# Kernel tuning notes

Measured on AMD Instinct MI355X. Metric: run time of the kernel, lower is better.

## Reference

```python
import jax, jax.numpy as jnp
import numpy as np

B, S, IN_DIM, P_DIM, H = 2, 2048, 1024, 512, 8
HD = P_DIM // H
N_PENTA = 1024
SCALES = (128, 256, 512)
K_NEIGH = max(16, min(int(S * 0.15), 128))  # adaptive window -> 128
SCALE = 1.0 / float(np.sqrt(HD))
EPS = 1e-5


def _ln(x, g, b):
    mu = jnp.mean(x, axis=-1, keepdims=True)
    var = jnp.mean((x - mu) ** 2, axis=-1, keepdims=True)
    return (x - mu) * jax.lax.rsqrt(var + EPS) * g + b


def setup_inputs() -> dict:
    key = jax.random.key(0)
    ks = list(jax.random.split(key, 6 + 2 * len(SCALES)))
    w = lambda k, shp: jax.random.normal(k, shp, jnp.float32) * 0.02
    inp = {
        'sequence_features': jax.random.normal(ks[0], (B, S, IN_DIM), jnp.float32),
        'shared_pentachora': jax.random.normal(ks[1], (N_PENTA, 5, P_DIM), jnp.float32),
        'shared_positions': jax.random.uniform(ks[2], (N_PENTA,), dtype=jnp.float32),
        'proj_W': w(ks[3], (IN_DIM, P_DIM)), 'proj_b': jnp.zeros((P_DIM,), jnp.float32),
        'ln_g': jnp.ones((P_DIM,), jnp.float32), 'ln_b': jnp.zeros((P_DIM,), jnp.float32),
        'qkv_W': w(ks[4], (P_DIM, 3 * P_DIM)), 'qkv_b': jnp.zeros((3 * P_DIM,), jnp.float32),
        'out_W': w(ks[5], (P_DIM, P_DIM)), 'out_b': jnp.zeros((P_DIM,), jnp.float32),
    }
    i = 6
    for s in SCALES:
        inp[f'w1_{s}'] = w(ks[i], (P_DIM, 2 * s)); inp[f'b1_{s}'] = jnp.zeros((2 * s,), jnp.float32)
        inp[f'g_{s}'] = jnp.ones((2 * s,), jnp.float32); inp[f'bb_{s}'] = jnp.zeros((2 * s,), jnp.float32)
        inp[f'w2_{s}'] = w(ks[i + 1], (2 * s, s)); inp[f'b2_{s}'] = jnp.zeros((s,), jnp.float32)
        i += 2
    return inp


def _attend_one(z_b, pos_b, qkv_W, qkv_b, out_W, out_b):
    # z_b: [S, P_DIM], pos_b: [S]
    qkv = (z_b @ qkv_W + qkv_b).reshape(S, 3, H, HD)
    q = jnp.transpose(qkv[:, 0], (1, 0, 2))  # [H, S, HD]
    k = jnp.transpose(qkv[:, 1], (1, 0, 2))
    v = jnp.transpose(qkv[:, 2], (1, 0, 2))
    dist = jnp.abs(pos_b[:, None] - pos_b[None, :])  # [S, S]
    _, routes = jax.lax.top_k(-dist, K_NEIGH)        # [S, K] nearest in Cantor space
    kg = k[:, routes, :]  # [H, S, K, HD] gathered keys
    vg = v[:, routes, :]
    scores = jnp.einsum('hqd,hqkd->hqk', q, kg) * SCALE
    attn = jax.nn.softmax(scores, axis=-1)
    out = jnp.einsum('hqk,hqkd->hqd', attn, vg)
    out = jnp.transpose(out, (1, 0, 2)).reshape(S, P_DIM)
    return out @ out_W + out_b


def reference(sequence_features, shared_pentachora, shared_positions, proj_W, proj_b, ln_g, ln_b, qkv_W, qkv_b, out_W, out_b, w1_128, b1_128, g_128, bb_128, w2_128, b2_128, w1_256, b1_256, g_256, bb_256, w2_256, b2_256, w1_512, b1_512, g_512, bb_512, w2_512, b2_512):
    # centroids from pentachora vertices, L2-normalized
    cent = shared_pentachora.mean(axis=1)
    cent = cent / jnp.clip(jnp.linalg.norm(cent, axis=-1, keepdims=True), 1e-12)
    # input projection -> LN -> GELU -> L2 normalize
    z = jax.nn.gelu(_ln(sequence_features @ proj_W + proj_b, ln_g, ln_b), approximate=False)
    z = z / jnp.clip(jnp.linalg.norm(z, axis=-1, keepdims=True), 1e-12)
    # match to opinion anchors, inherit Cantor positions
    anchor_ids = jnp.argmax(jnp.einsum('bnd,pd->bnp', z, cent), axis=-1)  # [B, S]
    cantor_positions = shared_positions[anchor_ids]  # [B, S]
    # per-sample geometric sparse attention (vmapped over batch)
    z_att = jax.vmap(_attend_one, in_axes=(0, 0, None, None, None, None))(
        z, cantor_positions, qkv_W, qkv_b, out_W, out_b)  # [B, S, P_DIM]
    pooled = z_att.mean(axis=1)  # [B, P_DIM] (no attention mask)
    scale_params = (
        (w1_128, b1_128, g_128, bb_128, w2_128, b2_128),
        (w1_256, b1_256, g_256, bb_256, w2_256, b2_256),
        (w1_512, b1_512, g_512, bb_512, w2_512, b2_512),
    )
    outs = []
    for (w1, b1, g, bb, w2, b2) in scale_params:
        h = jax.nn.gelu(_ln(pooled @ w1 + b1, g, bb), approximate=False)
        outs.append(h @ w2 + b2)
    return jnp.concatenate(outs, axis=-1)  # [B, 128+256+512] concatenated scale opinions
```

## Files before the change

### kernel.cpp

```cpp
#include <hip/hip_runtime.h>
#include <math.h>

#define DEV __device__ __forceinline__

static constexpr int S_LEN  = 2048;
static constexpr int IN_DIM = 1024;
static constexpr int P_DIM  = 512;
static constexpr int NHEAD  = 8;
static constexpr int HD     = 64;
static constexpr int KN     = 128;

typedef __attribute__((ext_vector_type(8))) short bf16x8;
typedef __attribute__((ext_vector_type(4))) float f32x4;

DEV float gelu_exact(float x) {
    return 0.5f * x * (1.0f + erff(x * 0.70710678118654752440f));
}

DEV short bf_hi(float x) {
    unsigned u = __float_as_uint(x);
    unsigned r = (u + 0x7fffu + ((u >> 16) & 1u)) >> 16;
    return (short)r;
}
DEV float bf_f(short h) { return __uint_as_float(((unsigned)(unsigned short)h) << 16); }

DEV float block_reduce_sum(float v, float* sm4) {
    #pragma unroll
    for (int off = 32; off; off >>= 1) v += __shfl_down(v, off, 64);
    int lane = threadIdx.x & 63, w = threadIdx.x >> 6;
    __syncthreads();
    if (lane == 0) sm4[w] = v;
    __syncthreads();
    return sm4[0] + sm4[1] + sm4[2] + sm4[3];
}

DEV float wave_sum(float v) {
    #pragma unroll
    for (int off = 32; off; off >>= 1) v += __shfl_xor(v, off, 64);
    return v;
}

DEV void wt_body(const float* __restrict__ W, short* __restrict__ WTh,
                 short* __restrict__ WTl, int K, int N, int bk, int bn,
                 float (*tile)[65]) {
    int t = threadIdx.x;
    int c = t & 63, r4 = t >> 6;
    #pragma unroll
    for (int i = 0; i < 16; i++) {
        int row = r4 + i * 4;
        tile[row][c] = W[(long)(bk * 64 + row) * N + bn * 64 + c];
    }
    __syncthreads();
    #pragma unroll
    for (int i = 0; i < 16; i++) {
        int n = r4 + i * 4;
        float v = tile[c][n];
        short h = bf_hi(v);
        long o = (long)(bn * 64 + n) * K + bk * 64 + c;
        WTh[o] = h;
        WTl[o] = bf_hi(v - bf_f(h));
    }
}

DEV void t32_body(const float* __restrict__ W, float* __restrict__ WT,
                  int K, int N, int bk, int bn, float (*tile)[65]) {
    int t = threadIdx.x;
    int c = t & 63, r4 = t >> 6;
    #pragma unroll
    for (int i = 0; i < 16; i++) {
        int row = r4 + i * 4;
        tile[row][c] = W[(long)(bk * 64 + row) * N + bn * 64 + c];
    }
    __syncthreads();
    #pragma unroll
    for (int i = 0; i < 16; i++) {
        int n = r4 + i * 4;
        WT[(long)(bn * 64 + n) * K + bk * 64 + c] = tile[c][n];
    }
}

__global__ __launch_bounds__(256) void k_prep(const float* __restrict__ penta,
                                              short* __restrict__ ch, short* __restrict__ cl,
                                              const float* __restrict__ projW,
                                              short* __restrict__ pjh, short* __restrict__ pjl,
                                              const float* __restrict__ qkvW,
                                              short* __restrict__ qkh, short* __restrict__ qkl,
                                              const float* __restrict__ seq,
                                              short* __restrict__ sh, short* __restrict__ sl,
                                              unsigned long long* __restrict__ rowkey,
                                              float* __restrict__ pooledZ,
                                              const float* __restrict__ outW, float* __restrict__ outWT,
                                              const float* __restrict__ w1_0,
                                              const float* __restrict__ w1_1,
                                              const float* __restrict__ w1_2, float* __restrict__ w1T,
                                              const float* __restrict__ w2_0,
                                              const float* __restrict__ w2_1,
                                              const float* __restrict__ w2_2, float* __restrict__ w2T) {
    __shared__ float tile[64][65];
    __shared__ float sm4[4];
    int blk = blockIdx.x, t = threadIdx.x;
    if (blk < 1024) {
        int p = blk;
        if (t < 4) rowkey[p * 4 + t] = 0ull;
        if (p < 4) pooledZ[p * 256 + t] = 0.f;
        float c0 = 0.f, c1 = 0.f;
        #pragma unroll
        for (int v = 0; v < 5; v++) {
            const float* row = penta + ((long)p * 5 + v) * P_DIM;
            c0 += row[t];
            c1 += row[t + 256];
        }
        c0 /= 5.0f; c1 /= 5.0f;
        float tot = block_reduce_sum(c0 * c0 + c1 * c1, sm4);
        float n = fmaxf(sqrtf(tot), 1e-12f);
        float v0 = c0 / n, v1 = c1 / n;
        short h0 = bf_hi(v0), h1 = bf_hi(v1);
        ch[p * P_DIM + t]       = h0;
        ch[p * P_DIM + t + 256] = h1;
        cl[p * P_DIM + t]       = bf_hi(v0 - bf_f(h0));
        cl[p * P_DIM + t + 256] = bf_hi(v1 - bf_f(h1));
    } else if (blk < 1152) {
        int id = blk - 1024;
        wt_body(projW, pjh, pjl, IN_DIM, P_DIM, id & 15, id >> 4, tile);
    } else if (blk < 1344) {
        int id = blk - 1152;
        wt_body(qkvW, qkh, qkl, P_DIM, 3 * P_DIM, id & 7, id >> 3, tile);
    } else if (blk < 2368) {
        long base = ((long)(blk - 1344) * 256 + t) * 16;
        #pragma unroll
        for (int u = 0; u < 4; u++) {
            float4 v = *(const float4*)(seq + base + u * 4);
            short h0 = bf_hi(v.x), h1 = bf_hi(v.y), h2 = bf_hi(v.z), h3 = bf_hi(v.w);
            *(short4*)(sh + base + u * 4) = make_short4(h0, h1, h2, h3);
            *(short4*)(sl + base + u * 4) =
                make_short4(bf_hi(v.x - bf_f(h0)), bf_hi(v.y - bf_f(h1)),
                            bf_hi(v.z - bf_f(h2)), bf_hi(v.w - bf_f(h3)));
        }
    } else if (blk < 2432) {
        int id = blk - 2368;
        t32_body(outW, outWT, 512, 512, id & 7, id >> 3, tile);
    } else if (blk < 2464) {
        int id = blk - 2432;
        t32_body(w1_0, w1T, 512, 256, id & 7, id >> 3, tile);
    } else if (blk < 2528) {
        int id = blk - 2464;
        t32_body(w1_1, w1T + 256 * 512, 512, 512, id & 7, id >> 3, tile);
    } else if (blk < 2656) {
        int id = blk - 2528;
        t32_body(w1_2, w1T + 768 * 512, 512, 1024, id & 7, id >> 3, tile);
    } else if (blk < 2664) {
        int id = blk - 2656;
        t32_body(w2_0, w2T, 256, 128, id & 3, id >> 2, tile);
    } else if (blk < 2696) {
        int id = blk - 2664;
        t32_body(w2_1, w2T + 32768, 512, 256, id & 7, id >> 3, tile);
    } else {
        int id = blk - 2696;
        t32_body(w2_2, w2T + 163840, 1024, 512, id & 15, id >> 4, tile);
    }
}

template <int BM, int K, int N, int EPI>
__global__ __launch_bounds__(256) void k_mm(const short* __restrict__ Ash,
                                            const short* __restrict__ Asl,
                                            const short* __restrict__ BTh,
                                            const short* __restrict__ BTl,
                                            const float* __restrict__ bias,
                                            float* __restrict__ C,
                                            unsigned long long* __restrict__ rowkey) {
    constexpr int TI  = BM / 32;
    constexpr int CA  = BM / 8;
    constexpr int NCH = 2 * CA + 32;
    __shared__ __align__(128) short AhS[BM * 64], AlS[BM * 64];
    __shared__ __align__(128) short BhS[128 * 64], BlS[128 * 64];
    int t = threadIdx.x;
    int lane = t & 63, wave = t >> 6;
    int wr = (wave >> 1) * (BM / 2), wc = (wave & 1) * 64;
    int m = lane & 15, quad = lane >> 4;
    int rb = blockIdx.x * BM, cb = blockIdx.y * 128;
    int r8 = lane >> 3, p8 = lane & 7;
    int sl = p8 ^ r8;

    f32x4 acc[TI][4];
    #pragma unroll
    for (int i = 0; i < TI; i++)
        #pragma unroll
        for (int j = 0; j < 4; j++) acc[i][j] = (f32x4){0.f, 0.f, 0.f, 0.f};

    for (int k0 = 0; k0 < K; k0 += 64) {
        __syncthreads();
        for (int c = wave; c < NCH; c += 4) {
            const short* src; short* dst;
            if (c < CA) {
                src = Ash + (long)(rb + c * 8 + r8) * K + k0 + sl * 8;
                dst = AhS + c * 512;
            } else if (c < 2 * CA) {
                int cc = c - CA;
                src = Asl + (long)(rb + cc * 8 + r8) * K + k0 + sl * 8;
                dst = AlS + cc * 512;
            } else if (c < 2 * CA + 16) {
                int cc = c - 2 * CA;
                src = BTh + (long)(cb + cc * 8 + r8) * K + k0 + sl * 8;
                dst = BhS + cc * 512;
            } else {
                int cc = c - 2 * CA - 16;
                src = BTl + (long)(cb + cc * 8 + r8) * K + k0 + sl * 8;
                dst = BlS + cc * 512;
            }
            __builtin_amdgcn_global_load_lds(
                (const __attribute__((address_space(1))) unsigned int*)src,
                (__attribute__((address_space(3))) unsigned int*)dst, 16, 0, 0);
        }
        __syncthreads();

        #pragma unroll
        for (int ks = 0; ks < 2; ks++) {
            int so = ((ks * 4 + quad) ^ (m & 7)) * 8;
            bf16x8 ah[TI], al[TI], bh[4], bl[4];
            #pragma unroll
            for (int i = 0; i < TI; i++) {
                int off = (wr + i * 16 + m) * 64 + so;
                ah[i] = *(const bf16x8*)(AhS + off);
                al[i] = *(const bf16x8*)(AlS + off);
            }
            #pragma unroll
            for (int j = 0; j < 4; j++) {
                int off = (wc + j * 16 + m) * 64 + so;
                bh[j] = *(const bf16x8*)(BhS + off);
                bl[j] = *(const bf16x8*)(BlS + off);
            }
            #pragma unroll
            for (int i = 0; i < TI; i++)
                #pragma unroll
                for (int j = 0; j < 4; j++) {
                    acc[i][j] = __builtin_amdgcn_mfma_f32_16x16x32_bf16(ah[i], bh[j], acc[i][j], 0, 0, 0);
                    acc[i][j] = __builtin_amdgcn_mfma_f32_16x16x32_bf16(ah[i], bl[j], acc[i][j], 0, 0, 0);
                    acc[i][j] = __builtin_amdgcn_mfma_f32_16x16x32_bf16(al[i], bh[j], acc[i][j], 0, 0, 0);
                }
        }
    }

    if (EPI == 0) {
        #pragma unroll
        for (int i = 0; i < TI; i++) {
            int gr0 = rb + wr + i * 16 + quad * 4;
            #pragma unroll
            for (int j = 0; j < 4; j++) {
                int gc = cb + wc + j * 16 + m;
                float bv = bias[gc];
                #pragma unroll
                for (int r = 0; r < 4; r++)
                    C[(long)(gr0 + r) * N + gc] = acc[i][j][r] + bv;
            }
        }
    } else {
        #pragma unroll
        for (int i = 0; i < TI; i++) {
            #pragma unroll
            for (int r = 0; r < 4; r++) {
                int gr = rb + wr + i * 16 + quad * 4 + r;
                float bv = acc[i][0][r];
                int bp = cb + wc + m;
                #pragma unroll
                for (int j = 1; j < 4; j++) {
                    float v = acc[i][j][r];
                    int p = cb + wc + j * 16 + m;
                    if (v > bv) { bv = v; bp = p; }
                }
                #pragma unroll
                for (int off = 1; off < 16; off <<= 1) {
                    float ov = __shfl_xor(bv, off, 64);
                    int op = __shfl_xor(bp, off, 64);
                    if (ov > bv || (ov == bv && op < bp)) { bv = ov; bp = op; }
                }
                if (m == 0) {
                    unsigned u = __float_as_uint(bv);
                    u = (u & 0x80000000u) ? ~u : (u | 0x80000000u);
                    unsigned long long key =
                        ((unsigned long long)u << 32) | (unsigned)(0xFFFFFFFFu - (unsigned)bp);
                    atomicMax(&rowkey[gr], key);
                }
            }
        }
    }
}

__global__ __launch_bounds__(256) void k_mmz(const short* __restrict__ Ash,
                                             const short* __restrict__ Asl,
                                             const short* __restrict__ Ch,
                                             const short* __restrict__ Cl,
                                             const short* __restrict__ Qh,
                                             const short* __restrict__ Ql,
                                             const float* __restrict__ bias,
                                             float* __restrict__ C,
                                             unsigned long long* __restrict__ rowkey) {
    constexpr int BM = 64, K = 512;
    constexpr int TI  = BM / 32;
    constexpr int CA  = BM / 8;
    constexpr int NCH = 2 * CA + 32;
    __shared__ __align__(128) short AhS[BM * 64], AlS[BM * 64];
    __shared__ __align__(128) short BhS[128 * 64], BlS[128 * 64];
    int t = threadIdx.x;
    int lane = t & 63, wave = t >> 6;
    int wr = (wave >> 1) * (BM / 2), wc = (wave & 1) * 64;
    int m = lane & 15, quad = lane >> 4;
    bool anchor = blockIdx.y < 8;
    const short* BTh = anchor ? Ch : Qh;
    const short* BTl = anchor ? Cl : Ql;
    int rb = blockIdx.x * BM;
    int cb = (anchor ? blockIdx.y : (blockIdx.y - 8)) * 128;
    int r8 = lane >> 3, p8 = lane & 7;
    int sl = p8 ^ r8;

    f32x4 acc[TI][4];
    #pragma unroll
    for (int i = 0; i < TI; i++)
        #pragma unroll
        for (int j = 0; j < 4; j++) acc[i][j] = (f32x4){0.f, 0.f, 0.f, 0.f};

    for (int k0 = 0; k0 < K; k0 += 64) {
        __syncthreads();
        for (int c = wave; c < NCH; c += 4) {
            const short* src; short* dst;
            if (c < CA) {
                src = Ash + (long)(rb + c * 8 + r8) * K + k0 + sl * 8;
                dst = AhS + c * 512;
            } else if (c < 2 * CA) {
                int cc = c - CA;
                src = Asl + (long)(rb + cc * 8 + r8) * K + k0 + sl * 8;
                dst = AlS + cc * 512;
            } else if (c < 2 * CA + 16) {
                int cc = c - 2 * CA;
                src = BTh + (long)(cb + cc * 8 + r8) * K + k0 + sl * 8;
                dst = BhS + cc * 512;
            } else {
                int cc = c - 2 * CA - 16;
                src = BTl + (long)(cb + cc * 8 + r8) * K + k0 + sl * 8;
                dst = BlS + cc * 512;
            }
            __builtin_amdgcn_global_load_lds(
                (const __attribute__((address_space(1))) unsigned int*)src,
                (__attribute__((address_space(3))) unsigned int*)dst, 16, 0, 0);
        }
        __syncthreads();

        #pragma unroll
        for (int ks = 0; ks < 2; ks++) {
            int so = ((ks * 4 + quad) ^ (m & 7)) * 8;
            bf16x8 ah[TI], al[TI], bh[4], bl[4];
            #pragma unroll
            for (int i = 0; i < TI; i++) {
                int off = (wr + i * 16 + m) * 64 + so;
                ah[i] = *(const bf16x8*)(AhS + off);
                al[i] = *(const bf16x8*)(AlS + off);
            }
            #pragma unroll
            for (int j = 0; j < 4; j++) {
                int off = (wc + j * 16 + m) * 64 + so;
                bh[j] = *(const bf16x8*)(BhS + off);
                bl[j] = *(const bf16x8*)(BlS + off);
            }
            #pragma unroll
            for (int i = 0; i < TI; i++)
                #pragma unroll
                for (int j = 0; j < 4; j++) {
                    acc[i][j] = __builtin_amdgcn_mfma_f32_16x16x32_bf16(ah[i], bh[j], acc[i][j], 0, 0, 0);
                    acc[i][j] = __builtin_amdgcn_mfma_f32_16x16x32_bf16(ah[i], bl[j], acc[i][j], 0, 0, 0);
                    acc[i][j] = __builtin_amdgcn_mfma_f32_16x16x32_bf16(al[i], bh[j], acc[i][j], 0, 0, 0);
                }
        }
    }

    if (!anchor) {
        #pragma unroll
        for (int i = 0; i < TI; i++) {
            int gr0 = rb + wr + i * 16 + quad * 4;
            #pragma unroll
            for (int j = 0; j < 4; j++) {
                int gc = cb + wc + j * 16 + m;
                float bv = bias[gc];
                #pragma unroll
                for (int r = 0; r < 4; r++)
                    C[(long)(gr0 + r) * 1536 + gc] = acc[i][j][r] + bv;
            }
        }
    } else {
        #pragma unroll
        for (int i = 0; i < TI; i++) {
            #pragma unroll
            for (int r = 0; r < 4; r++) {
                int gr = rb + wr + i * 16 + quad * 4 + r;
                float bv = acc[i][0][r];
                int bp = cb + wc + m;
                #pragma unroll
                for (int j = 1; j < 4; j++) {
                    float v = acc[i][j][r];
                    int p = cb + wc + j * 16 + m;
                    if (v > bv) { bv = v; bp = p; }
                }
                #pragma unroll
                for (int off = 1; off < 16; off <<= 1) {
                    float ov = __shfl_xor(bv, off, 64);
                    int op = __shfl_xor(bp, off, 64);
                    if (ov > bv || (ov == bv && op < bp)) { bv = ov; bp = op; }
                }
                if (m == 0) {
                    unsigned u = __float_as_uint(bv);
                    u = (u & 0x80000000u) ? ~u : (u | 0x80000000u);
                    unsigned long long key =
                        ((unsigned long long)u << 32) | (unsigned)(0xFFFFFFFFu - (unsigned)bp);
                    atomicMax(&rowkey[gr], key);
                }
            }
        }
    }
}

__global__ __launch_bounds__(256) void k_ln_gelu_norm(const float* __restrict__ Zin,
                                                      const float* __restrict__ g,
                                                      const float* __restrict__ b,
                                                      short* __restrict__ z_h,
                                                      short* __restrict__ z_l) {
    long row = blockIdx.x;
    int t = threadIdx.x;
    __shared__ float sm4[4];
    float x0 = Zin[row * P_DIM + t], x1 = Zin[row * P_DIM + t + 256];
    float mu = block_reduce_sum(x0 + x1, sm4) * (1.0f / P_DIM);
    float d0 = x0 - mu, d1 = x1 - mu;
    float var = block_reduce_sum(d0 * d0 + d1 * d1, sm4) * (1.0f / P_DIM);
    float rs = 1.0f / sqrtf(var + 1e-5f);
    float y0 = gelu_exact(d0 * rs * g[t] + b[t]);
    float y1 = gelu_exact(d1 * rs * g[t + 256] + b[t + 256]);
    float nn = block_reduce_sum(y0 * y0 + y1 * y1, sm4);
    float n = fmaxf(sqrtf(nn), 1e-12f);
    float v0 = y0 / n, v1 = y1 / n;
    short h0 = bf_hi(v0), h1 = bf_hi(v1);
    z_h[row * P_DIM + t]       = h0;
    z_h[row * P_DIM + t + 256] = h1;
    z_l[row * P_DIM + t]       = bf_hi(v0 - bf_f(h0));
    z_l[row * P_DIM + t + 256] = bf_hi(v1 - bf_f(h1));
}

__global__ __launch_bounds__(256) void k_rank(const unsigned long long* __restrict__ rowkey,
                                              const float* __restrict__ spos,
                                              int* __restrict__ order,
                                              float* __restrict__ pos_srt) {
    int b = blockIdx.y, t = threadIdx.x;
    __shared__ unsigned long long key[2048];
    for (int u = 0; u < 8; u++) {
        int i = t + u * 256;
        unsigned p = 0xFFFFFFFFu - (unsigned)(rowkey[b * 2048 + i] & 0xFFFFFFFFull);
        key[i] = (((unsigned long long)__float_as_uint(spos[p])) << 32) | (unsigned)i;
    }
    __syncthreads();
    int i = blockIdx.x * 256 + t;
    unsigned long long ki = key[i];
    int rank = 0;
    #pragma unroll 8
    for (int j = 0; j < 2048; j++) rank += (key[j] < ki) ? 1 : 0;
    order[b * 2048 + rank]   = i;
    pos_srt[b * 2048 + rank] = __uint_as_float((unsigned)(ki >> 32));
}

__global__ __launch_bounds__(256) void k_routeskv(const float* __restrict__ pos_srt,
                                                  const int* __restrict__ order,
                                                  unsigned long long* __restrict__ bmG,
                                                  uint2* __restrict__ bounds,
                                                  const float* __restrict__ qkv,
                                                  short* __restrict__ Ks_h,
                                                  short* __restrict__ Ks_l,
                                                  short* __restrict__ Vt_h) {
    __shared__ __align__(16) char smem[12288];
    int blk0 = blockIdx.x, t = threadIdx.x;
    if (blk0 < 1024) {
        float* ps = (float*)smem;
        unsigned short* tk = (unsigned short*)(smem + 8192);
        int blk = blk0;
        int b = blk >> 9;
        int lane = t & 63, wave = t >> 6;
        int r = (blk & 511) * 4 + wave;
        for (int u = 0; u < 8; u++) {
            int i = t + u * 256;
            ps[i] = pos_srt[b * 2048 + i];
            tk[i] = (unsigned short)order[b * 2048 + i];
        }
        __syncthreads();

        float pi = ps[r];
        float T = 3e38f;
        #pragma unroll
        for (int a2 = 0; a2 < 2; a2++) {
            int a = lane + a2 * 64;
            int jl = r - a, jr = r + 127 - a;
            if (jl >= 0 && jr <= 2047) {
                float dl = (a > 0)   ? (pi - ps[jl]) : 0.f;
                float dr = (a < 127) ? (ps[jr] - pi) : 0.f;
                T = fminf(T, fmaxf(dl, dr));
            }
        }
        #pragma unroll
        for (int off = 1; off < 64; off <<= 1) T = fminf(T, __shfl_xor(T, off, 64));

        int lo = 0, hi = r;
        while (lo < hi) { int mid = (lo + hi) >> 1; if (pi - ps[mid] <= T) hi = mid; else lo = mid + 1; }
        int mn = lo;
        lo = r; hi = 2047;
        while (lo < hi) { int mid = (lo + hi + 1) >> 1; if (ps[mid] - pi <= T) lo = mid; else hi = mid - 1; }
        int mx = lo;
        int Ls, Rs;
        if (T > 0.f) {
            lo = 0; hi = r;
            while (lo < hi) { int mid = (lo + hi) >> 1; if (pi - ps[mid] < T) hi = mid; else lo = mid + 1; }
            Ls = lo;
            lo = r; hi = 2047;
            while (lo < hi) { int mid = (lo + hi + 1) >> 1; if (ps[mid] - pi < T) lo = mid; else hi = mid - 1; }
            Rs = lo;
        } else { Ls = r + 1; Rs = r - 1; }

        int cnt_strict = (Rs >= Ls) ? (Rs - Ls + 1) : 0;
        int need = 128 - cnt_strict;
        int l0a, l0b, r0a, r0b;
        if (cnt_strict > 0) { l0a = mn; l0b = Ls - 1; r0a = Rs + 1; r0b = mx; }
        else                { l0a = mn; l0b = mx;     r0a = 1;      r0b = 0; }
        int nL = (l0b >= l0a) ? (l0b - l0a + 1) : 0;
        int nR = (r0b >= r0a) ? (r0b - r0a + 1) : 0;
        int tiecount = nL + nR;

        int X = 65535;
        if (need < tiecount) {
            int lo2 = 0, hi2 = 2047;
            while (lo2 < hi2) {
                int mid = (lo2 + hi2) >> 1;
                int cnt = 0;
                for (int e = lane; e < tiecount; e += 64) {
                    int j = (e < nL) ? (l0a + e) : (r0a + e - nL);
                    cnt += (tk[j] <= mid) ? 1 : 0;
                }
                #pragma unroll
                for (int off = 1; off < 64; off <<= 1) cnt += __shfl_xor(cnt, off, 64);
                if (cnt >= need) hi2 = mid; else lo2 = mid + 1;
            }
            X = lo2;
        }

        int qlo_loc = 1 << 30, qhi_loc = -1;
        if (lane < 32) {
            unsigned long long bits = 0;
            int j0 = lane << 6, j1 = j0 + 63;
            if (cnt_strict > 0) {
                int a0 = max(Ls, j0), a1 = min(Rs, j1);
                if (a0 <= a1) {
                    int s = a0 - j0, e = a1 - j0;
                    unsigned long long msk = (e - s == 63) ? ~0ull
                                           : (((1ull << (e - s + 1)) - 1) << s);
                    bits |= msk;
                }
            }
            int a0 = max(l0a, j0), a1 = min(l0b, j1);
            for (int j = a0; j <= a1; j++) if (tk[j] <= X) bits |= 1ull << (j - j0);
            a0 = max(r0a, j0); a1 = min(r0b, j1);
            for (int j = a0; j <= a1; j++) if (tk[j] <= X) bits |= 1ull << (j - j0);
            if (bits) {
                qlo_loc = j0 + __builtin_ctzll(bits);
                qhi_loc = j0 + 63 - __builtin_clzll(bits);
            }
            bmG[((long)(b * 2048 + r)) * 32 + lane] = bits;
        }
        #pragma unroll
        for (int off = 1; off < 64; off <<= 1) {
            qlo_loc = min(qlo_loc, __shfl_xor(qlo_loc, off, 64));
            qhi_loc = max(qhi_loc, __shfl_xor(qhi_loc, off, 64));
        }
        if (lane == 0)
            bounds[b * 2048 + r] = make_uint2((unsigned)qlo_loc, (unsigned)qhi_loc);
    } else if (blk0 < 1536) {
        int blk = blk0 - 1024;
        int b = blk >> 8, bx = blk & 255;
        int lr = t >> 5;
        int seg = t & 31;
        int rank = bx * 8 + lr;
        int tok = order[b * 2048 + rank];
        const float4* src = (const float4*)qkv + (long)(b * 2048 + tok) * 384 + 128 + seg * 4;
        long dsto = (long)(b * 2048 + rank) * 512 + seg * 16;
        #pragma unroll
        for (int u = 0; u < 4; u++) {
            float4 v = src[u];
            short h0 = bf_hi(v.x), h1 = bf_hi(v.y), h2 = bf_hi(v.z), h3 = bf_hi(v.w);
            *(short4*)(Ks_h + dsto + u * 4) = make_short4(h0, h1, h2, h3);
            *(short4*)(Ks_l + dsto + u * 4) =
                make_short4(bf_hi(v.x - bf_f(h0)), bf_hi(v.y - bf_f(h1)),
                            bf_hi(v.z - bf_f(h2)), bf_hi(v.w - bf_f(h3)));
        }
    } else {
        short (*tile)[72] = (short(*)[72])smem;
        int id = blk0 - 1536;
        int rt = id & 31, dt = (id >> 5) & 7, b = id >> 8;
        int lr = t >> 2;
        int q4 = t & 3;
        int tok = order[b * 2048 + rt * 64 + lr];
        const float4* src = (const float4*)qkv + (long)(b * 2048 + tok) * 384 + 256 + dt * 16;
        #pragma unroll
        for (int u = 0; u < 4; u++) {
            float4 v = src[q4 + u * 4];
            int d0 = (q4 + u * 4) * 4;
            tile[d0 + 0][lr] = bf_hi(v.x);
            tile[d0 + 1][lr] = bf_hi(v.y);
            tile[d0 + 2][lr] = bf_hi(v.z);
            tile[d0 + 3][lr] = bf_hi(v.w);
        }
        __syncthreads();
        int d = t >> 2, c4 = t & 3;
        long o = ((long)(b * 512 + dt * 64 + d)) * 2048 + rt * 64 + c4 * 16;
        #pragma unroll
        for (int j = 0; j < 4; j++)
            *(short4*)(Vt_h + o + j * 4) = make_short4(tile[d][c4 * 16 + j * 4 + 0],
                                                       tile[d][c4 * 16 + j * 4 + 1],
                                                       tile[d][c4 * 16 + j * 4 + 2],
                                                       tile[d][c4 * 16 + j * 4 + 3]);
    }
}

__global__ __launch_bounds__(256) void k_attn(const float* __restrict__ qkv,
                                              const int* __restrict__ order,
                                              const unsigned long long* __restrict__ bmG,
                                              const uint2* __restrict__ bounds,
                                              const short* __restrict__ Ks_h,
                                              const short* __restrict__ Ks_l,
                                              const short* __restrict__ Vt_h,
                                              float* __restrict__ pooledZ) {
    __shared__ __align__(16) char smem[17280];
    short* Pt = (short*)smem;
    unsigned short* cm = (unsigned short*)(smem + 10240);
    float* Opart = (float*)smem;
    float2* ml = (float2*)(smem + 16384);
    int* sh_tok = (int*)(smem + 16896);
    int* sh_lohi = (int*)(smem + 16960);
    float2* sc = (float2*)(smem + 16968);

    int gb = blockIdx.x;
    int b  = gb >> 9;
    int qg = (gb >> 2) & 127;
    int hp = gb & 3;
    int h0 = hp * 2;
    int r0 = qg * 16;
    int t = threadIdx.x;
    int lane = t & 63, wave = t >> 6;
    int rh = wave & 1, hs = wave >> 1;
    int key = lane & 15, quad = lane >> 4;

    const float4* qkvF4 = (const float4*)qkv;

    if (t < 16) sh_tok[t] = order[b * 2048 + r0 + t];
    if (t == 0) { sh_lohi[0] = 1 << 30; sh_lohi[1] = 0; }
    #pragma unroll
    for (int u = 0; u < 8; u++) {
        int e = t + u * 256;
        int c = e >> 4, q = e & 15;
        cm[c * 16 + q] = (unsigned short)(
            (bmG[((long)(b * 2048 + r0 + q)) * 32 + (c >> 2)] >> ((c & 3) * 16)) & 0xFFFF);
    }
    __syncthreads();
    if (t < 16) {
        uint2 bd = bounds[b * 2048 + r0 + t];
        atomicMin(&sh_lohi[0], (int)bd.x);
        atomicMax(&sh_lohi[1], (int)bd.y);
    }

    bf16x8 qh[2], ql[2];
    {
        long tq = (long)(b * 2048 + sh_tok[key]) * 384;
        #pragma unroll
        for (int ks = 0; ks < 2; ks++) {
            float4 v0 = qkvF4[tq + (h0 + hs) * 16 + ks * 8 + quad * 2];
            float4 v1 = qkvF4[tq + (h0 + hs) * 16 + ks * 8 + quad * 2 + 1];
            float vv[8] = {v0.x, v0.y, v0.z, v0.w, v1.x, v1.y, v1.z, v1.w};
            #pragma unroll
            for (int j = 0; j < 8; j++) {
                short hb = bf_hi(vv[j]);
                qh[ks][j] = hb;
                ql[ks][j] = bf_hi(vv[j] - bf_f(hb));
            }
        }
    }
    __syncthreads();
    int lo = sh_lohi[0] & ~63, hi = sh_lohi[1] + 1;

    float mrow[4], lrow[4];
    f32x4 Ont[4];
    #pragma unroll
    for (int r = 0; r < 4; r++) { mrow[r] = -1e30f; lrow[r] = 0.f; }
    #pragma unroll
    for (int nt = 0; nt < 4; nt++) Ont[nt] = (f32x4){0.f, 0.f, 0.f, 0.f};

    short* PtH = Pt + wave * 1280;
    short* PtL = PtH + 640;

    int hd = h0 + hs;
    long kbase = ((long)b * 2048) * 512 + hd * 64 + quad * 8;
    long vbase = ((long)(b * 512 + hd * 64 + key)) * 2048;

    for (int c0 = lo; c0 < hi; c0 += 64) {
        int cb = c0 + rh * 32;
        if (cb >= hi) continue;
        int ch0 = cb >> 4;
        unsigned long long m0 = *(const unsigned long long*)(cm + ch0 * 16 + quad * 4);
        unsigned long long m1 = (ch0 + 1 < 128)
            ? *(const unsigned long long*)(cm + (ch0 + 1) * 16 + quad * 4) : 0ull;
        if (!__any((m0 | m1) != 0ull)) continue;

        long kr0 = kbase + (long)(cb + key) * 512;
        long kr1 = kbase + (long)(cb + 16 + key) * 512;

        f32x4 S0 = (f32x4){0.f,0.f,0.f,0.f}, S1 = (f32x4){0.f,0.f,0.f,0.f};
        __builtin_amdgcn_s_setprio(1);
        #pragma unroll
        for (int ks = 0; ks < 2; ks++) {
            bf16x8 b0h = *(const bf16x8*)(Ks_h + kr0 + ks * 32);
            bf16x8 b0l = *(const bf16x8*)(Ks_l + kr0 + ks * 32);
            bf16x8 b1h = *(const bf16x8*)(Ks_h + kr1 + ks * 32);
            bf16x8 b1l = *(const bf16x8*)(Ks_l + kr1 + ks * 32);
            S0 = __builtin_amdgcn_mfma_f32_16x16x32_bf16(qh[ks], b0h, S0, 0, 0, 0);
            S0 = __builtin_amdgcn_mfma_f32_16x16x32_bf16(qh[ks], b0l, S0, 0, 0, 0);
            S0 = __builtin_amdgcn_mfma_f32_16x16x32_bf16(ql[ks], b0h, S0, 0, 0, 0);
            S1 = __builtin_amdgcn_mfma_f32_16x16x32_bf16(qh[ks], b1h, S1, 0, 0, 0);
            S1 = __builtin_amdgcn_mfma_f32_16x16x32_bf16(qh[ks], b1l, S1, 0, 0, 0);
            S1 = __builtin_amdgcn_mfma_f32_16x16x32_bf16(ql[ks], b1h, S1, 0, 0, 0);
        }
        __builtin_amdgcn_s_setprio(0);
        float s0[4], s1[4], p0[4], p1[4];
        unsigned bit0[4], bit1[4];
        #pragma unroll
        for (int r = 0; r < 4; r++) {
            bit0[r] = (unsigned)((m0 >> (r * 16 + key)) & 1);
            bit1[r] = (unsigned)((m1 >> (r * 16 + key)) & 1);
            s0[r] = bit0[r] ? S0[r] * 0.125f : -1e30f;
            s1[r] = bit1[r] ? S1[r] * 0.125f : -1e30f;
        }
        #pragma unroll
        for (int r = 0; r < 4; r++) {
            float cmax = fmaxf(s0[r], s1[r]);
            cmax = fmaxf(cmax, __shfl_xor(cmax, 1, 64));
            cmax = fmaxf(cmax, __shfl_xor(cmax, 2, 64));
            cmax = fmaxf(cmax, __shfl_xor(cmax, 4, 64));
            cmax = fmaxf(cmax, __shfl_xor(cmax, 8, 64));
            float mn = fmaxf(mrow[r], cmax);
            float alpha = __expf(mrow[r] - mn);
            mrow[r] = mn;
            p0[r] = bit0[r] ? __expf(s0[r] - mn) : 0.f;
            p1[r] = bit1[r] ? __expf(s1[r] - mn) : 0.f;
            float rs = p0[r] + p1[r];
            rs += __shfl_xor(rs, 1, 64);
            rs += __shfl_xor(rs, 2, 64);
            rs += __shfl_xor(rs, 4, 64);
            rs += __shfl_xor(rs, 8, 64);
            lrow[r] = lrow[r] * alpha + rs;
            #pragma unroll
            for (int nt = 0; nt < 4; nt++) Ont[nt][r] *= alpha;
        }
        #pragma unroll
        for (int r = 0; r < 4; r++) {
            short ha = bf_hi(p0[r]);
            PtH[(quad * 4 + r) * 40 + key] = ha;
            PtL[(quad * 4 + r) * 40 + key] = bf_hi(p0[r] - bf_f(ha));
            short hb = bf_hi(p1[r]);
            PtH[(quad * 4 + r) * 40 + 16 + key] = hb;
            PtL[(quad * 4 + r) * 40 + 16 + key] = bf_hi(p1[r] - bf_f(hb));
        }
        bf16x8 pfh = *(const bf16x8*)(PtH + key * 40 + quad * 8);
        bf16x8 pfl = *(const bf16x8*)(PtL + key * 40 + quad * 8);
        __builtin_amdgcn_s_setprio(1);
        #pragma unroll
        for (int nt = 0; nt < 4; nt++) {
            bf16x8 vf = *(const bf16x8*)(Vt_h + vbase + (long)nt * 16 * 2048
                                         + cb + quad * 8);
            Ont[nt] = __builtin_amdgcn_mfma_f32_16x16x32_bf16(pfh, vf, Ont[nt], 0, 0, 0);
            Ont[nt] = __builtin_amdgcn_mfma_f32_16x16x32_bf16(pfl, vf, Ont[nt], 0, 0, 0);
        }
        __builtin_amdgcn_s_setprio(0);
    }

    if (key == 0) {
        #pragma unroll
        for (int r = 0; r < 4; r++)
            ml[(rh * 2 + hs) * 16 + quad * 4 + r] = make_float2(mrow[r], lrow[r]);
    }
    __syncthreads();
    #pragma unroll
    for (int nt = 0; nt < 4; nt++)
        #pragma unroll
        for (int r = 0; r < 4; r++)
            Opart[rh * 2048 + (quad * 4 + r) * 128 + hs * 64 + nt * 16 + key] = Ont[nt][r];

    if (t < 32) {
        int q = t >> 1, hs2 = t & 1;
        float2 a = ml[(0 * 2 + hs2) * 16 + q];
        float2 c = ml[(1 * 2 + hs2) * 16 + q];
        float M = fmaxf(a.x, c.x);
        float w0 = __expf(a.x - M), w1 = __expf(c.x - M);
        float inv = 1.0f / fmaxf(a.y * w0 + c.y * w1, 1e-37f);
        sc[hs2 * 16 + q] = make_float2(w0 * inv, w1 * inv);
    }
    __syncthreads();

    if (t < 128) {
        int d = t, hs2 = d >> 6;
        float s = 0.f;
        #pragma unroll
        for (int q = 0; q < 16; q++) {
            float2 w = sc[hs2 * 16 + q];
            s += Opart[q * 128 + d] * w.x + Opart[2048 + q * 128 + d] * w.y;
        }
        atomicAdd(&pooledZ[b * P_DIM + h0 * HD + d], s);
    }
}

__global__ __launch_bounds__(256) void k_gemv_opool(const float* __restrict__ pooledZ,
                                                    const float* __restrict__ outWT,
                                                    const float* __restrict__ outb,
                                                    float* __restrict__ pooled) {
    int b = blockIdx.y, t = threadIdx.x;
    int lane = t & 63, w = t >> 6;
    __shared__ float pz[P_DIM];
    pz[t]       = pooledZ[b * P_DIM + t];
    pz[t + 256] = pooledZ[b * P_DIM + t + 256];
    __syncthreads();
    int c = blockIdx.x * 4 + w;
    const float* wp = outWT + (long)c * 512;
    float acc = 0.f;
    #pragma unroll
    for (int i = 0; i < 8; i++) acc = fmaf(pz[lane + i * 64], wp[lane + i * 64], acc);
    acc = wave_sum(acc);
    if (lane == 0) pooled[b * P_DIM + c] = acc + (float)S_LEN * outb[c];
}

__global__ __launch_bounds__(256) void k_gemv_fc1(const float* __restrict__ pooled,
                                                  const float* __restrict__ w1T,
                                                  const float* __restrict__ b1_0,
                                                  const float* __restrict__ b1_1,
                                                  const float* __restrict__ b1_2,
                                                  float* __restrict__ h) {
    int b = blockIdx.y, t = threadIdx.x;
    int lane = t & 63, w = t >> 6;
    __shared__ float pl[P_DIM];
    pl[t]       = pooled[b * P_DIM + t]       * (1.0f / S_LEN);
    pl[t + 256] = pooled[b * P_DIM + t + 256] * (1.0f / S_LEN);
    __syncthreads();
    int c = blockIdx.x * 4 + w;
    const float* wp = w1T + (long)c * 512;
    float acc = 0.f;
    #pragma unroll
    for (int i = 0; i < 8; i++) acc = fmaf(pl[lane + i * 64], wp[lane + i * 64], acc);
    acc = wave_sum(acc);
    if (lane == 0) {
        float bb = (c < 256) ? b1_0[c] : (c < 768) ? b1_1[c - 256] : b1_2[c - 768];
        h[(long)b * 1792 + c] = acc + bb;
    }
}

__global__ __launch_bounds__(256) void k_gemv_fc2(const float* __restrict__ h,
                                                  const float* __restrict__ w2T,
                                                  const float* __restrict__ b2_0,
                                                  const float* __restrict__ b2_1,
                                                  const float* __restrict__ b2_2,
                                                  float* __restrict__ out) {
    int b = blockIdx.y, t = threadIdx.x;
    int lane = t & 63, w = t >> 6;
    __shared__ float hh[1792];
    for (int u = 0; u < 7; u++) hh[t + u * 256] = h[(long)b * 1792 + t + u * 256];
    __syncthreads();
    int c = blockIdx.x * 4 + w;
    const float* wp; const float* hp; int s2; float bb;
    if (c < 128)      { wp = w2T + (long)c * 256;                hp = hh;       s2 = 256;  bb = b2_0[c]; }
    else if (c < 384) { wp = w2T + 32768 + (long)(c - 128) * 512;  hp = hh + 256; s2 = 512;  bb = b2_1[c - 128]; }
    else              { wp = w2T + 163840 + (long)(c - 384) * 1024; hp = hh + 768; s2 = 1024; bb = b2_2[c - 384]; }
    float acc = 0.f;
    for (int i = lane; i < s2; i += 64) acc = fmaf(hp[i], wp[i], acc);
    acc = wave_sum(acc);
    if (lane == 0) out[b * 896 + c] = acc + bb;
}

__global__ __launch_bounds__(256) void k_exp_ln(float* __restrict__ h,
                                                const float* __restrict__ g0, const float* __restrict__ bb0,
                                                const float* __restrict__ g1, const float* __restrict__ bb1,
                                                const float* __restrict__ g2, const float* __restrict__ bb2) {
    int e = blockIdx.x, b = blockIdx.y, t = threadIdx.x;
    __shared__ float sm4[4];
    const int offs[3] = {0, 256, 768};
    const int ns[3]   = {256, 512, 1024};
    const float* gs[3]  = {g0, g1, g2};
    const float* bbs[3] = {bb0, bb1, bb2};
    int n = ns[e];
    float* hp = h + (long)b * 1792 + offs[e];
    const float* g = gs[e]; const float* bb = bbs[e];

    float x[4];
    float loc = 0.f;
    for (int u = 0; u < 4; u++) {
        int j = t + u * 256;
        x[u] = (j < n) ? hp[j] : 0.f;
        loc += x[u];
    }
    float mu = block_reduce_sum(loc, sm4) / (float)n;
    loc = 0.f;
    for (int u = 0; u < 4; u++) {
        int j = t + u * 256;
        if (j < n) { float d = x[u] - mu; loc += d * d; }
    }
    float var = block_reduce_sum(loc, sm4) / (float)n;
    float rs = 1.0f / sqrtf(var + 1e-5f);
    for (int u = 0; u < 4; u++) {
        int j = t + u * 256;
        if (j < n) hp[j] = gelu_exact((x[u] - mu) * rs * g[j] + bb[j]);
    }
}

extern "C" void kernel_launch(void* const* d_in, const int* in_sizes, int n_in,
                              void* d_out, int out_size, void* d_ws, size_t ws_size,
                              hipStream_t stream) {
    const float* seq   = (const float*)d_in[0];
    const float* penta = (const float*)d_in[1];
    const float* spos  = (const float*)d_in[2];
    const float* projW = (const float*)d_in[3];
    const float* projb = (const float*)d_in[4];
    const float* lng   = (const float*)d_in[5];
    const float* lnb   = (const float*)d_in[6];
    const float* qkvW  = (const float*)d_in[7];
    const float* qkvb  = (const float*)d_in[8];
    const float* outW  = (const float*)d_in[9];
    const float* outb  = (const float*)d_in[10];

    float* ws      = (float*)d_ws;
    float* z_pre   = ws;
    short* z_h     = (short*)(z_pre + 2097152);
    short* z_l     = z_h + 2097152;
    float* qkv     = (float*)(z_l + 2097152);
    float* pooledZ = qkv + 6291456;
    float* pooled  = pooledZ + 4096;
    float* hbuf    = pooled + 1024;
    unsigned long long* rowkey = (unsigned long long*)(hbuf + 4096);
    float* pos_srt = (float*)(rowkey + 4096);
    int*   order   = (int*)(pos_srt + 4096);
    uint2* bounds  = (uint2*)(order + 4096);
    unsigned long long* bmG = (unsigned long long*)(bounds + 4096);
    short* cent_h  = (short*)(bmG + 131072);
    short* cent_l  = cent_h + 524288;
    short* pjWT_h  = cent_l + 524288;
    short* pjWT_l  = pjWT_h + 524288;
    short* qkWT_h  = pjWT_l + 524288;
    short* qkWT_l  = qkWT_h + 786432;
    float* outWT   = (float*)(qkWT_l + 786432);
    float* w1T     = outWT + 262144;
    float* w2T     = w1T + 917504;

    short* seq_h = (short*)qkv;
    short* seq_l = seq_h + 4194304;
    short* Ks_h = (short*)z_pre;
    short* Ks_l = Ks_h + 2097152;
    short* Vt_h = cent_h;

    k_prep<<<2824, 256, 0, stream>>>(penta, cent_h, cent_l,
                                     projW, pjWT_h, pjWT_l,
                                     qkvW, qkWT_h, qkWT_l,
                                     seq, seq_h, seq_l,
                                     rowkey, pooledZ,
                                     outW, outWT,
                                     (const float*)d_in[11],
                                     (const float*)d_in[17],
                                     (const float*)d_in[23], w1T,
                                     (const float*)d_in[15],
                                     (const float*)d_in[21],
                                     (const float*)d_in[27], w2T);

    { dim3 g(64, 4);  k_mm<64, IN_DIM, P_DIM, 0><<<g, 256, 0, stream>>>(
          seq_h, seq_l, pjWT_h, pjWT_l, projb, z_pre, nullptr); }
    k_ln_gelu_norm<<<4096, 256, 0, stream>>>(z_pre, lng, lnb, z_h, z_l);

    { dim3 g(64, 20); k_mmz<<<g, 256, 0, stream>>>(
          z_h, z_l, cent_h, cent_l, qkWT_h, qkWT_l, qkvb, qkv, rowkey); }

    { dim3 g(8, 2);   k_rank<<<g, 256, 0, stream>>>(rowkey, spos, order, pos_srt); }
    k_routeskv<<<2048, 256, 0, stream>>>(pos_srt, order, bmG, bounds,
                                         qkv, Ks_h, Ks_l, Vt_h);
    k_attn<<<1024, 256, 0, stream>>>(qkv, order, bmG, bounds,
                                     Ks_h, Ks_l, Vt_h, pooledZ);

    { dim3 g(128, 2); k_gemv_opool<<<g, 256, 0, stream>>>(pooledZ, outWT, outb, pooled); }
    { dim3 g(448, 2); k_gemv_fc1<<<g, 256, 0, stream>>>(pooled, w1T,
        (const float*)d_in[12], (const float*)d_in[18], (const float*)d_in[24], hbuf); }
    { dim3 g(3, 2);   k_exp_ln<<<g, 256, 0, stream>>>(hbuf,
        (const float*)d_in[13], (const float*)d_in[14],
        (const float*)d_in[19], (const float*)d_in[20],
        (const float*)d_in[25], (const float*)d_in[26]); }
    { dim3 g(224, 2); k_gemv_fc2<<<g, 256, 0, stream>>>(hbuf, w2T,
        (const float*)d_in[16], (const float*)d_in[22], (const float*)d_in[28],
        (float*)d_out); }
}
```

Baseline: 324.3 us.

## Fuse tail GEMV/LN kernels into one cooperative kernel with grid syncs

```diff
diff --git a/kernel.cpp b/kernel.cpp
--- a/kernel.cpp
+++ b/kernel.cpp
@@ -1,4 +1,5 @@
 #include <hip/hip_runtime.h>
+#include <hip/hip_cooperative_groups.h>
 #include <math.h>
 
 #define DEV __device__ __forceinline__
@@ -814,103 +815,101 @@
     }
 }
 
-__global__ __launch_bounds__(256) void k_gemv_opool(const float* __restrict__ pooledZ,
-                                                    const float* __restrict__ outWT,
-                                                    const float* __restrict__ outb,
-                                                    float* __restrict__ pooled) {
-    int b = blockIdx.y, t = threadIdx.x;
+__global__ __launch_bounds__(256) void k_tailco(
+        const float* __restrict__ pooledZ,
+        const float* __restrict__ outWT, const float* __restrict__ outb,
+        const float* __restrict__ w1T,
+        const float* __restrict__ b1_0, const float* __restrict__ b1_1,
+        const float* __restrict__ b1_2,
+        const float* __restrict__ g_0,  const float* __restrict__ bb_0,
+        const float* __restrict__ g_1,  const float* __restrict__ bb_1,
+        const float* __restrict__ g_2,  const float* __restrict__ bb_2,
+        const float* __restrict__ w2T,
+        const float* __restrict__ b2_0, const float* __restrict__ b2_1,
+        const float* __restrict__ b2_2,
+        float* __restrict__ pooled, float* __restrict__ h,
+        float* __restrict__ out) {
+    cooperative_groups::grid_group gg = cooperative_groups::this_grid();
+    __shared__ float buf[1792];
+    __shared__ float sm4[4];
+    int bx = blockIdx.x, b = blockIdx.y, t = threadIdx.x;
     int lane = t & 63, w = t >> 6;
-    __shared__ float pz[P_DIM];
-    pz[t]       = pooledZ[b * P_DIM + t];
-    pz[t + 256] = pooledZ[b * P_DIM + t + 256];
-    __syncthreads();
-    int c = blockIdx.x * 4 + w;
-    const float* wp = outWT + (long)c * 512;
-    float acc = 0.f;
-    #pragma unroll
-    for (int i = 0; i < 8; i++) acc = fmaf(pz[lane + i * 64], wp[lane + i * 64], acc);
-    acc = wave_sum(acc);
-    if (lane == 0) pooled[b * P_DIM + c] = acc + (float)S_LEN * outb[c];
-}
-
-__global__ __launch_bounds__(256) void k_gemv_fc1(const float* __restrict__ pooled,
-                                                  const float* __restrict__ w1T,
-                                                  const float* __restrict__ b1_0,
-                                                  const float* __restrict__ b1_1,
-                                                  const float* __restrict__ b1_2,
-                                                  float* __restrict__ h) {
-    int b = blockIdx.y, t = threadIdx.x;
-    int lane = t & 63, w = t >> 6;
-    __shared__ float pl[P_DIM];
-    pl[t]       = pooled[b * P_DIM + t]       * (1.0f / S_LEN);
-    pl[t + 256] = pooled[b * P_DIM + t + 256] * (1.0f / S_LEN);
-    __syncthreads();
-    int c = blockIdx.x * 4 + w;
-    const float* wp = w1T + (long)c * 512;
-    float acc = 0.f;
-    #pragma unroll
-    for (int i = 0; i < 8; i++) acc = fmaf(pl[lane + i * 64], wp[lane + i * 64], acc);
-    acc = wave_sum(acc);
-    if (lane == 0) {
-        float bb = (c < 256) ? b1_0[c] : (c < 768) ? b1_1[c - 256] : b1_2[c - 768];
-        h[(long)b * 1792 + c] = acc + bb;
-    }
-}
-
-__global__ __launch_bounds__(256) void k_gemv_fc2(const float* __restrict__ h,
-                                                  const float* __restrict__ w2T,
-                                                  const float* __restrict__ b2_0,
-                                                  const float* __restrict__ b2_1,
-                                                  const float* __restrict__ b2_2,
-                                                  float* __restrict__ out) {
-    int b = blockIdx.y, t = threadIdx.x;
-    int lane = t & 63, w = t >> 6;
-    __shared__ float hh[1792];
-    for (int u = 0; u < 7; u++) hh[t + u * 256] = h[(long)b * 1792 + t + u * 256];
-    __syncthreads();
-    int c = blockIdx.x * 4 + w;
-    const float* wp; const float* hp; int s2; float bb;
-    if (c < 128)      { wp = w2T + (long)c * 256;                hp = hh;       s2 = 256;  bb = b2_0[c]; }
-    else if (c < 384) { wp = w2T + 32768 + (long)(c - 128) * 512;  hp = hh + 256; s2 = 512;  bb = b2_1[c - 128]; }
-    else              { wp = w2T + 163840 + (long)(c - 384) * 1024; hp = hh + 768; s2 = 1024; bb = b2_2[c - 384]; }
-    float acc = 0.f;
-    for (int i = lane; i < s2; i += 64) acc = fmaf(hp[i], wp[i], acc);
-    acc = wave_sum(acc);
-    if (lane == 0) out[b * 896 + c] = acc + bb;
-}
-
-__global__ __launch_bounds__(256) void k_exp_ln(float* __restrict__ h,
-                                                const float* __restrict__ g0, const float* __restrict__ bb0,
-                                                const float* __restrict__ g1, const float* __restrict__ bb1,
-                                                const float* __restrict__ g2, const float* __restrict__ bb2) {
-    int e = blockIdx.x, b = blockIdx.y, t = threadIdx.x;
-    __shared__ float sm4[4];
-    const int offs[3] = {0, 256, 768};
-    const int ns[3]   = {256, 512, 1024};
-    const float* gs[3]  = {g0, g1, g2};
-    const float* bbs[3] = {bb0, bb1, bb2};
-    int n = ns[e];
-    float* hp = h + (long)b * 1792 + offs[e];
-    const float* g = gs[e]; const float* bb = bbs[e];
-
-    float x[4];
-    float loc = 0.f;
-    for (int u = 0; u < 4; u++) {
-        int j = t + u * 256;
-        x[u] = (j < n) ? hp[j] : 0.f;
-        loc += x[u];
-    }
-    float mu = block_reduce_sum(loc, sm4) / (float)n;
-    loc = 0.f;
-    for (int u = 0; u < 4; u++) {
-        int j = t + u * 256;
-        if (j < n) { float d = x[u] - mu; loc += d * d; }
-    }
-    float var = block_reduce_sum(loc, sm4) / (float)n;
-    float rs = 1.0f / sqrtf(var + 1e-5f);
-    for (int u = 0; u < 4; u++) {
-        int j = t + u * 256;
-        if (j < n) hp[j] = gelu_exact((x[u] - mu) * rs * g[j] + bb[j]);
+
+    if (bx < 128) {
+        buf[t]       = pooledZ[b * P_DIM + t];
+        buf[t + 256] = pooledZ[b * P_DIM + t + 256];
+        __syncthreads();
+        int c = bx * 4 + w;
+        const float* wp = outWT + (long)c * 512;
+        float acc = 0.f;
+        #pragma unroll
+        for (int i = 0; i < 8; i++) acc = fmaf(buf[lane + i * 64], wp[lane + i * 64], acc);
+        acc = wave_sum(acc);
+        if (lane == 0) pooled[b * P_DIM + c] = acc + (float)S_LEN * outb[c];
+    }
+    gg.sync();
+
+    {
+        buf[t]       = pooled[b * P_DIM + t]       * (1.0f / S_LEN);
+        buf[t + 256] = pooled[b * P_DIM + t + 256] * (1.0f / S_LEN);
+        __syncthreads();
+        int c = bx * 4 + w;
+        const float* wp = w1T + (long)c * 512;
+        float acc = 0.f;
+        #pragma unroll
+        for (int i = 0; i < 8; i++) acc = fmaf(buf[lane + i * 64], wp[lane + i * 64], acc);
+        acc = wave_sum(acc);
+        if (lane == 0) {
+            float bb = (c < 256) ? b1_0[c] : (c < 768) ? b1_1[c - 256] : b1_2[c - 768];
+            h[(long)b * 1792 + c] = acc + bb;
+        }
+    }
+    gg.sync();
+
+    if (bx < 3) {
+        int e = bx;
+        const int offs[3] = {0, 256, 768};
+        const int ns[3]   = {256, 512, 1024};
+        const float* gs[3]  = {g_0, g_1, g_2};
+        const float* bbs[3] = {bb_0, bb_1, bb_2};
+        int n = ns[e];
+        float* hp = h + (long)b * 1792 + offs[e];
+        const float* g = gs[e]; const float* bb = bbs[e];
+
+        float x[4];
+        float loc = 0.f;
+        for (int u = 0; u < 4; u++) {
+            int j = t + u * 256;
+            x[u] = (j < n) ? hp[j] : 0.f;
+            loc += x[u];
+        }
+        float mu = block_reduce_sum(loc, sm4) / (float)n;
+        loc = 0.f;
+        for (int u = 0; u < 4; u++) {
+            int j = t + u * 256;
+            if (j < n) { float d = x[u] - mu; loc += d * d; }
+        }
+        float var = block_reduce_sum(loc, sm4) / (float)n;
+        float rs = 1.0f / sqrtf(var + 1e-5f);
+        for (int u = 0; u < 4; u++) {
+            int j = t + u * 256;
+            if (j < n) hp[j] = gelu_exact((x[u] - mu) * rs * g[j] + bb[j]);
+        }
+    }
+    gg.sync();
+
+    if (bx < 224) {
+        for (int u = 0; u < 7; u++) buf[t + u * 256] = h[(long)b * 1792 + t + u * 256];
+        __syncthreads();
+        int c = bx * 4 + w;
+        const float* wp; const float* hp2; int s2; float bb;
+        if (c < 128)      { wp = w2T + (long)c * 256;                  hp2 = buf;       s2 = 256;  bb = b2_0[c]; }
+        else if (c < 384) { wp = w2T + 32768 + (long)(c - 128) * 512;  hp2 = buf + 256; s2 = 512;  bb = b2_1[c - 128]; }
+        else              { wp = w2T + 163840 + (long)(c - 384) * 1024; hp2 = buf + 768; s2 = 1024; bb = b2_2[c - 384]; }
+        float acc = 0.f;
+        for (int i = lane; i < s2; i += 64) acc = fmaf(hp2[i], wp[i], acc);
+        acc = wave_sum(acc);
+        if (lane == 0) out[b * 896 + c] = acc + bb;
     }
 }
 
@@ -984,14 +983,32 @@
     k_attn<<<1024, 256, 0, stream>>>(qkv, order, bmG, bounds,
                                      Ks_h, Ks_l, Vt_h, pooledZ);
 
-    { dim3 g(128, 2); k_gemv_opool<<<g, 256, 0, stream>>>(pooledZ, outWT, outb, pooled); }
-    { dim3 g(448, 2); k_gemv_fc1<<<g, 256, 0, stream>>>(pooled, w1T,
-        (const float*)d_in[12], (const float*)d_in[18], (const float*)d_in[24], hbuf); }
-    { dim3 g(3, 2);   k_exp_ln<<<g, 256, 0, stream>>>(hbuf,
-        (const float*)d_in[13], (const float*)d_in[14],
-        (const float*)d_in[19], (const float*)d_in[20],
-        (const float*)d_in[25], (const float*)d_in[26]); }
-    { dim3 g(224, 2); k_gemv_fc2<<<g, 256, 0, stream>>>(hbuf, w2T,
-        (const float*)d_in[16], (const float*)d_in[22], (const float*)d_in[28],
-        (float*)d_out); }
-}
+    {
+        const float* b1_0 = (const float*)d_in[12];
+        const float* b1_1 = (const float*)d_in[18];
+        const float* b1_2 = (const float*)d_in[24];
+        const float* g_0  = (const float*)d_in[13];
+        const float* bb_0 = (const float*)d_in[14];
+        const float* g_1  = (const float*)d_in[19];
+        const float* bb_1 = (const float*)d_in[20];
+        const float* g_2  = (const float*)d_in[25];
+        const float* bb_2 = (const float*)d_in[26];
+        const float* b2_0 = (const float*)d_in[16];
+        const float* b2_1 = (const float*)d_in[22];
+        const float* b2_2 = (const float*)d_in[28];
+        float* outp = (float*)d_out;
+        const float* pooledZc = pooledZ;
+        const float* outWTc = outWT;
+        const float* w1Tc = w1T;
+        const float* w2Tc = w2T;
+        void* args[] = {
+            (void*)&pooledZc, (void*)&outWTc, (void*)&outb,
+            (void*)&w1Tc, (void*)&b1_0, (void*)&b1_1, (void*)&b1_2,
+            (void*)&g_0, (void*)&bb_0, (void*)&g_1, (void*)&bb_1,
+            (void*)&g_2, (void*)&bb_2,
+            (void*)&w2Tc, (void*)&b2_0, (void*)&b2_1, (void*)&b2_2,
+            (void*)&pooled, (void*)&hbuf, (void*)&outp };
+        hipLaunchCooperativeKernel((void*)k_tailco, dim3(448, 2), dim3(256),
+                                   args, 0, stream);
+    }
+}
```

New measurement: 654.7 us. 102% more time.
